# Optimization experiments

Measured on AMD Instinct MI355X. Metric: run time of the kernel, lower is better.

The kernel has to match this reference:

```python
import jax, jax.numpy as jnp
import numpy as np

N_POINTS = 2_000_000
N_BATCH = 8


def cart2polar(xyz):
    rho = jnp.sqrt(xyz[:, 0] ** 2 + xyz[:, 1] ** 2)
    phi = jnp.arctan2(xyz[:, 1], xyz[:, 0])
    return jnp.stack((rho, phi, xyz[:, 2]), axis=1)


def setup_inputs() -> dict:
    key = jax.random.key(0)
    k1, k2, k3, k4 = jax.random.split(key, 4)
    xy = jax.random.uniform(k1, (N_POINTS, 2), minval=-50.0, maxval=50.0)
    z = jax.random.uniform(k2, (N_POINTS, 1), minval=-4.0, maxval=2.0)
    inten = jax.random.uniform(k3, (N_POINTS, 1))
    points = jnp.concatenate([xy, z, inten], axis=1)  # [N, 4]
    batch_idx = jnp.sort(jax.random.randint(k4, (N_POINTS,), 0, N_BATCH)).astype(jnp.int32)
    coors_range_xyz = jnp.array([[0.0, 50.0], [-np.pi, np.pi], [-4.0, 2.0]], dtype=jnp.float32)
    spatial_shape = np.array([480, 360, 32])  # static
    scale_list = np.array([2, 4, 1])          # module appends 1; static
    return dict(points=points, batch_idx=batch_idx,
                coors_range_xyz=coors_range_xyz,
                spatial_shape=spatial_shape, scale_list=scale_list)


def _unique_rows(bxyz, dims):
    # Encode [b, gx, gy, gz] rows into a single int32 key (max 8*480*360*32 ~ 44M).
    key = ((bxyz[:, 0] * dims[0] + bxyz[:, 1]) * dims[1] + bxyz[:, 2]) * dims[2] + bxyz[:, 3]
    order = jnp.argsort(key)
    sk = key[order]
    flags = jnp.concatenate([jnp.ones((1,), bool), sk[1:] != sk[:-1]])
    rank = jnp.cumsum(flags.astype(jnp.int32)) - 1          # unique-id per sorted row
    inv = jnp.zeros_like(rank).at[order].set(rank)           # inverse map, like torch.unique
    # first occurrence of each unique row (all rows with same rank are identical)
    unq = jnp.zeros_like(bxyz).at[rank].set(bxyz[order])     # padded to [N, 4]
    num_unique = rank[-1] + 1
    return unq, inv, num_unique


def reference(points, batch_idx, coors_range_xyz, spatial_shape, scale_list):
    pc = points[:, :3]
    xyz_pol = cart2polar(pc)
    lo = coors_range_xyz[:, 0]
    hi = coors_range_xyz[:, 1]
    crop = hi - lo
    ss_np = np.asarray(spatial_shape)
    outs = []
    for scale in [int(s) for s in np.asarray(scale_list)]:
        cells = jnp.asarray(np.ceil(ss_np / scale) - 1.0, dtype=xyz_pol.dtype)
        grid = jnp.floor((jnp.clip(xyz_pol, lo, hi) - lo) / crop * cells).astype(jnp.int32)
        bxyz = jnp.concatenate([batch_idx[:, None].astype(jnp.int32), grid], axis=1)  # [N,4]
        dims = np.ceil(ss_np / scale).astype(np.int64)
        unq, inv, num = _unique_rows(bxyz, dims)
        # reorder unique coords as [b, z, y, x], cast int32 (torch: unq[:, [0,3,2,1]])
        coors = jnp.concatenate([unq[:, 0:1], unq[:, 3:4], unq[:, 2:3], unq[:, 1:2]], axis=1).astype(jnp.int32)
        outs.extend([bxyz, inv, coors, num])
    return tuple(outs)
```

## Files before the change

kernel.cpp:

```cpp
#include <hip/hip_runtime.h>
#include <cstdint>

#define DI __device__ __forceinline__

constexpr int NPTS       = 2000000;
constexpr int STRIDE_OUT = 18000001;
constexpr int OFF_INV    = 8000000;
constexpr int OFF_COORS  = 10000000;
constexpr int OFF_NUM    = 18000000;

constexpr int R2W  = 172800;
constexpr int R4W  = 21600;
constexpr int R1W  = 1382400;
constexpr int RW0  = 0;
constexpr int RW1  = R2W;
constexpr int RW2  = R2W + R4W;
constexpr int WTOT = R2W + R4W + R1W;
constexpr int NB1  = (WTOT + 1023) / 1024;
constexpr int J2   = 8;

constexpr int NBLK_INV   = (NPTS + 255) / 256;
constexpr int NBLK_COORS = (WTOT + 255) / 256;
constexpr int NBLK_TAIL  = (3 * NPTS + 255) / 256;

DI float fmul_s(float a, float b){ float r; asm("v_mul_f32 %0, %1, %2" : "=v"(r) : "v"(a), "v"(b)); return r; }
DI float fadd_s(float a, float b){ float r; asm("v_add_f32 %0, %1, %2" : "=v"(r) : "v"(a), "v"(b)); return r; }

DI void compute_keys(float x, float y, float z, int b, int (&key)[3], int (&g0)[3], int (&g1)[3], int (&g2)[3]) {
  const float PI_F     = 3.14159265358979323846f;
  const float TWO_PI_F = 6.28318530717958647692f;
  float rho = sqrtf(fadd_s(fmul_s(x, x), fmul_s(y, y)));
  float phi = atan2f(y, x);
  float tr = (fminf(fmaxf(rho, 0.0f), 50.0f) - 0.0f) / 50.0f;
  float tp = (fminf(fmaxf(phi, -PI_F), PI_F) + PI_F) / TWO_PI_F;
  float tz = (fminf(fmaxf(z, -4.0f), 2.0f) + 4.0f) / 6.0f;
  constexpr float C0[3] = {239.f, 119.f, 479.f};
  constexpr float C1[3] = {179.f,  89.f, 359.f};
  constexpr float C2[3] = { 15.f,   7.f,  31.f};
  constexpr int   D0[3] = {240, 120, 480};
  constexpr int   D1[3] = {180,  90, 360};
  constexpr int   D2[3] = { 16,   8,  32};
  #pragma unroll
  for (int s = 0; s < 3; ++s) {
    int a0 = (int)floorf(tr * C0[s]);
    int a1 = (int)floorf(tp * C1[s]);
    int a2 = (int)floorf(tz * C2[s]);
    g0[s] = a0; g1[s] = a1; g2[s] = a2;
    key[s] = ((b * D0[s] + a0) * D1[s] + a1) * D2[s] + a2;
  }
}

DI int lower_bound(const int* __restrict__ a, int n, int v) {
  int lo = 0, hi = n;
  while (lo < hi) { int m = (lo + hi) >> 1; if (a[m] < v) lo = m + 1; else hi = m; }
  return lo;
}

__global__ __launch_bounds__(256) void pass_points(const float4* __restrict__ pts,
                                                   const int* __restrict__ batch, int n,
                                                   int* __restrict__ keys,
                                                   int* __restrict__ out) {
  int i = blockIdx.x * 256 + threadIdx.x;
  if (i >= n) return;
  float4 p = pts[i];
  int b = batch[i];
  int key[3], g0[3], g1[3], g2[3];
  compute_keys(p.x, p.y, p.z, b, key, g0, g1, g2);
  #pragma unroll
  for (int s = 0; s < 3; ++s)
    *reinterpret_cast<int4*>(out + s * STRIDE_OUT + i * 4) = make_int4(b, g0[s], g1[s], g2[s]);
  keys[i] = key[0]; keys[n + i] = key[1]; keys[2 * n + i] = key[2];
}

__global__ __launch_bounds__(1024) void hist_all(const int* __restrict__ batch,
                                                 const int* __restrict__ keys, int n,
                                                 uint32_t* __restrict__ rep2s,
                                                 uint32_t* __restrict__ rep4s,
                                                 uint32_t* __restrict__ rep1s, int j1) {
  alignas(16) __shared__ uint32_t bmA[21600];
  alignas(16) __shared__ uint32_t bmB[2700];
  int t = threadIdx.x;
  if ((int)blockIdx.x < 64) {
    int bv = blockIdx.x >> 3, j = blockIdx.x & 7;
    for (int w = t * 4; w < 21600; w += 4096) *reinterpret_cast<uint4*>(bmA + w) = make_uint4(0,0,0,0);
    for (int w = t; w < 2700; w += 1024) bmB[w] = 0;
    __syncthreads();
    int lo = lower_bound(batch, n, bv);
    int hi = lower_bound(batch, n, bv + 1);
    int sz = hi - lo;
    int s = lo + (int)((long long)sz * j / J2);
    int e = lo + (int)((long long)sz * (j + 1) / J2);
    const int* k0 = keys;
    const int* k1 = keys + n;
    for (int i = s + t; i < e; i += 1024) {
      int ink2 = k0[i] - bv * 691200;
      int ink4 = k1[i] - bv * 86400;
      atomicOr(&bmA[ink2 >> 5], 1u << (ink2 & 31));
      atomicOr(&bmB[ink4 >> 5], 1u << (ink4 & 31));
    }
    __syncthreads();
    uint32_t* d2 = rep2s + (size_t)j * R2W + bv * 21600;
    uint32_t* d4 = rep4s + (size_t)j * R4W + bv * 2700;
    for (int w = t * 4; w < 21600; w += 4096) *reinterpret_cast<uint4*>(d2 + w) = *reinterpret_cast<uint4*>(bmA + w);
    for (int w = t * 4; w < 2700; w += 4096) *reinterpret_cast<uint4*>(d4 + w) = *reinterpret_cast<uint4*>(bmB + w);
  } else {
    int idx = blockIdx.x - 64;
    int j = idx >> 6;
    int slice = idx & 63;
    int bv = slice >> 3, r = slice & 7;
    for (int w = t * 4; w < 21600; w += 4096) *reinterpret_cast<uint4*>(bmA + w) = make_uint4(0,0,0,0);
    __syncthreads();
    int lo = lower_bound(batch, n, bv);
    int hi = lower_bound(batch, n, bv + 1);
    int sz = hi - lo;
    int s = lo + (int)((long long)sz * j / j1);
    int e = lo + (int)((long long)sz * (j + 1) / j1);
    const int* k2 = keys + 2 * n;
    int base = bv * 5529600 + r * 691200;
    for (int i = s + t; i < e; i += 1024) {
      int rel = k2[i] - base;
      if ((unsigned)rel < 691200u) atomicOr(&bmA[rel >> 5], 1u << (rel & 31));
    }
    __syncthreads();
    uint32_t* d = rep1s + (size_t)j * R1W + (size_t)slice * 21600;
    for (int w = t * 4; w < 21600; w += 4096) *reinterpret_cast<uint4*>(d + w) = *reinterpret_cast<uint4*>(bmA + w);
  }
}

DI uint4 merged_words(int base, const uint32_t* __restrict__ rep2s,
                      const uint32_t* __restrict__ rep4s,
                      const uint32_t* __restrict__ rep1s, int j1) {
  uint4 acc = make_uint4(0, 0, 0, 0);
  if (base < RW1) {
    #pragma unroll
    for (int c = 0; c < J2; ++c) {
      uint4 w = *reinterpret_cast<const uint4*>(rep2s + (size_t)c * R2W + base);
      acc.x |= w.x; acc.y |= w.y; acc.z |= w.z; acc.w |= w.w;
    }
  } else if (base < RW2) {
    int l = base - RW1;
    #pragma unroll
    for (int c = 0; c < J2; ++c) {
      uint4 w = *reinterpret_cast<const uint4*>(rep4s + (size_t)c * R4W + l);
      acc.x |= w.x; acc.y |= w.y; acc.z |= w.z; acc.w |= w.w;
    }
  } else {
    int l = base - RW2;
    for (int c = 0; c < j1; ++c) {
      uint4 w = *reinterpret_cast<const uint4*>(rep1s + (size_t)c * R1W + l);
      acc.x |= w.x; acc.y |= w.y; acc.z |= w.z; acc.w |= w.w;
    }
  }
  return acc;
}

__global__ __launch_bounds__(256) void scanA(const uint32_t* __restrict__ rep2s,
                                             const uint32_t* __restrict__ rep4s,
                                             const uint32_t* __restrict__ rep1s, int j1,
                                             uint32_t* __restrict__ bits,
                                             uint32_t* __restrict__ blockSums) {
  __shared__ uint32_t lds[256];
  int t = threadIdx.x;
  int base = blockIdx.x * 1024 + t * 4;
  uint32_t s = 0;
  if (base < WTOT) {
    uint4 m = merged_words(base, rep2s, rep4s, rep1s, j1);
    *reinterpret_cast<uint4*>(bits + base) = m;
    s = __popc(m.x) + __popc(m.y) + __popc(m.z) + __popc(m.w);
  }
  lds[t] = s; __syncthreads();
  for (int off = 128; off > 0; off >>= 1) { if (t < off) lds[t] += lds[t + off]; __syncthreads(); }
  if (t == 0) blockSums[blockIdx.x] = lds[0];
}

__global__ __launch_bounds__(256) void scanB(uint32_t* __restrict__ blockSums,
                                             uint32_t* __restrict__ totals, int nb) {
  __shared__ uint32_t lds[256];
  int t = threadIdx.x;
  uint32_t local[7]; uint32_t sum = 0;
  #pragma unroll
  for (int k = 0; k < 7; ++k) { int idx = t * 7 + k; uint32_t v = (idx < nb) ? blockSums[idx] : 0u; local[k] = v; sum += v; }
  lds[t] = sum; __syncthreads();
  for (int off = 1; off < 256; off <<= 1) {
    uint32_t x = (t >= off) ? lds[t - off] : 0u; __syncthreads();
    lds[t] += x; __syncthreads();
  }
  uint32_t run = lds[t] - sum;
  #pragma unroll
  for (int k = 0; k < 7; ++k) { int idx = t * 7 + k; if (idx < nb) blockSums[idx] = run; run += local[k]; }
  if (t == 255) totals[0] = run;
}

__global__ __launch_bounds__(256) void scanC(const uint32_t* __restrict__ bits,
                                             const uint32_t* __restrict__ blockSums,
                                             uint2* __restrict__ pairs) {
  __shared__ uint32_t lds[256];
  int t = threadIdx.x;
  int base = blockIdx.x * 1024 + t * 4;
  uint32_t b[4] = {0,0,0,0}; uint32_t c[4]; uint32_t sum = 0;
  if (base < WTOT) {
    uint4 w = *reinterpret_cast<const uint4*>(bits + base);
    b[0] = w.x; b[1] = w.y; b[2] = w.z; b[3] = w.w;
  }
  #pragma unroll
  for (int k = 0; k < 4; ++k) { c[k] = __popc(b[k]); sum += c[k]; }
  lds[t] = sum; __syncthreads();
  for (int off = 1; off < 256; off <<= 1) {
    uint32_t x = (t >= off) ? lds[t - off] : 0u; __syncthreads();
    lds[t] += x; __syncthreads();
  }
  uint32_t excl = lds[t] - sum + blockSums[blockIdx.x];
  if (base < WTOT) {
    #pragma unroll
    for (int k = 0; k < 4; ++k) { pairs[base + k] = make_uint2(b[k], excl); excl += c[k]; }
  }
}

template <int S>
DI void coors_word(int wi_local, uint32_t bits, uint32_t rank, int* __restrict__ coors) {
  constexpr int D0[3] = {240, 120, 480};
  constexpr int D1[3] = {180,  90, 360};
  constexpr int D2[3] = { 16,   8,  32};
  int keybase = wi_local * 32;
  while (bits) {
    int j = __builtin_ctz(bits);
    bits &= bits - 1;
    int key = keybase + j;
    int gz = key & (D2[S] - 1);
    int r  = key / D2[S];
    int q  = r / D1[S];
    int gy = r - q * D1[S];
    int bq = q / D0[S];
    int gx = q - bq * D0[S];
    *reinterpret_cast<int4*>(coors + (size_t)rank * 4) = make_int4(bq, gz, gy, gx);
    ++rank;
  }
}

__global__ __launch_bounds__(256) void epilogue(int n, const uint2* __restrict__ pairs,
                                                const uint32_t* __restrict__ totals,
                                                const int* __restrict__ keys,
                                                int* __restrict__ out) {
  int b = blockIdx.x;
  int t = threadIdx.x;
  if (b < NBLK_INV) {
    int i = b * 256 + t;
    if (i >= n) return;
    int key[3] = { keys[i], keys[n + i], keys[2 * n + i] };
    constexpr int RW[3] = {RW0, RW1, RW2};
    #pragma unroll
    for (int s = 0; s < 3; ++s) {
      uint2 pr = pairs[RW[s] + (key[s] >> 5)];
      uint32_t base = pr.y - ((s == 0) ? 0u : pairs[RW[s]].y);
      int rank = (int)(base + __popc(pr.x & ((1u << (key[s] & 31)) - 1u)));
      out[s * STRIDE_OUT + OFF_INV + i] = rank;
    }
  } else if (b < NBLK_INV + NBLK_COORS) {
    int wi = (b - NBLK_INV) * 256 + t;
    if (wi >= WTOT) return;
    uint2 pr = pairs[wi];
    if (!pr.x) return;
    if (wi < RW1) {
      coors_word<0>(wi, pr.x, pr.y, out + 0 * STRIDE_OUT + OFF_COORS);
    } else if (wi < RW2) {
      coors_word<1>(wi - RW1, pr.x, pr.y - pairs[RW1].y, out + 1 * STRIDE_OUT + OFF_COORS);
    } else {
      coors_word<2>(wi - RW2, pr.x, pr.y - pairs[RW2].y, out + 2 * STRIDE_OUT + OFF_COORS);
    }
  } else {
    int idx = (b - NBLK_INV - NBLK_COORS) * 256 + t;
    int s = 0, i = idx;
    if (i >= 2 * n)      { s = 2; i -= 2 * n; }
    else if (i >= n)     { s = 1; i -= n; }
    if (idx >= 3 * n) return;
    uint32_t lo = (s == 0) ? 0u : pairs[(s == 1) ? RW1 : RW2].y;
    uint32_t hi = (s == 0) ? pairs[RW1].y : (s == 1) ? pairs[RW2].y : totals[0];
    uint32_t num = hi - lo;
    if (i == 0) out[s * STRIDE_OUT + OFF_NUM] = (int)num;
    if ((uint32_t)i >= num)
      *reinterpret_cast<int4*>(out + s * STRIDE_OUT + OFF_COORS + (size_t)i * 4) = make_int4(0, 0, 0, 0);
  }
}

extern "C" void kernel_launch(void* const* d_in, const int* in_sizes, int n_in,
                              void* d_out, int out_size, void* d_ws, size_t ws_size,
                              hipStream_t stream) {
  const float4* pts   = (const float4*)d_in[0];
  const int*    batch = (const int*)d_in[1];
  int n = in_sizes[1];
  int* out = (int*)d_out;

  size_t base_words = (size_t)J2 * R2W + (size_t)J2 * R4W + (size_t)WTOT +
                      2 * (size_t)WTOT + NB1 + 16 + (size_t)3 * n;
  int j1 = 4;
  while (j1 > 1 && (base_words + (size_t)j1 * R1W) * 4 > ws_size) j1 >>= 1;

  uint32_t* rep2s     = (uint32_t*)d_ws;
  uint32_t* rep4s     = rep2s + (size_t)J2 * R2W;
  uint32_t* rep1s     = rep4s + (size_t)J2 * R4W;
  uint32_t* bits      = rep1s + (size_t)j1 * R1W;
  uint2*    pairs     = (uint2*)(bits + WTOT);
  uint32_t* blockSums = (uint32_t*)(pairs + WTOT);
  uint32_t* totals    = blockSums + NB1;
  int*      keys      = (int*)(totals + 16);

  int nblk = (n + 255) / 256;
  pass_points<<<nblk, 256, 0, stream>>>(pts, batch, n, keys, out);
  hist_all<<<64 + 64 * j1, 1024, 0, stream>>>(batch, keys, n, rep2s, rep4s, rep1s, j1);
  scanA<<<NB1, 256, 0, stream>>>(rep2s, rep4s, rep1s, j1, bits, blockSums);
  scanB<<<1, 256, 0, stream>>>(blockSums, totals, NB1);
  scanC<<<NB1, 256, 0, stream>>>(bits, blockSums, pairs);
  epilogue<<<NBLK_INV + NBLK_COORS + NBLK_TAIL, 256, 0, stream>>>(n, pairs, totals, keys, out);
}
```

Before: 373.3 us.

## Defer bxyz writes to epilogue, drop scanB, retile scale-1 histogram

The first pass now writes only the packed keys. The epilogue decodes the per-point [b,gx,gy,gz] rows from those keys, so the first kernel no longer writes 96 MB of coordinate output. The single-block scanB is removed: each scanC block sums the preceding block totals itself, and the final count comes from the last pair. The scale-1 histogram uses 6 larger LDS slices per batch with a fixed 4-way split, giving 256 blocks total; this changes occupancy and the number of redundant key scans.

```diff
diff --git a/kernel.cpp b/kernel.cpp
--- a/kernel.cpp
+++ b/kernel.cpp
@@ -18,6 +18,10 @@
 constexpr int WTOT = R2W + R4W + R1W;
 constexpr int NB1  = (WTOT + 1023) / 1024;
 constexpr int J2   = 8;
+constexpr int P1   = 6;
+constexpr int J1   = 4;
+constexpr int S1W  = 28800;
+constexpr int S1BITS = S1W * 32;
 
 constexpr int NBLK_INV   = (NPTS + 255) / 256;
 constexpr int NBLK_COORS = (WTOT + 255) / 256;
@@ -26,7 +30,7 @@
 DI float fmul_s(float a, float b){ float r; asm("v_mul_f32 %0, %1, %2" : "=v"(r) : "v"(a), "v"(b)); return r; }
 DI float fadd_s(float a, float b){ float r; asm("v_add_f32 %0, %1, %2" : "=v"(r) : "v"(a), "v"(b)); return r; }
 
-DI void compute_keys(float x, float y, float z, int b, int (&key)[3], int (&g0)[3], int (&g1)[3], int (&g2)[3]) {
+DI void compute_keys(float x, float y, float z, int b, int (&key)[3]) {
   const float PI_F     = 3.14159265358979323846f;
   const float TWO_PI_F = 6.28318530717958647692f;
   float rho = sqrtf(fadd_s(fmul_s(x, x), fmul_s(y, y)));
@@ -45,7 +49,6 @@
     int a0 = (int)floorf(tr * C0[s]);
     int a1 = (int)floorf(tp * C1[s]);
     int a2 = (int)floorf(tz * C2[s]);
-    g0[s] = a0; g1[s] = a1; g2[s] = a2;
     key[s] = ((b * D0[s] + a0) * D1[s] + a1) * D2[s] + a2;
   }
 }
@@ -56,19 +59,14 @@
   return lo;
 }
 
-__global__ __launch_bounds__(256) void pass_points(const float4* __restrict__ pts,
-                                                   const int* __restrict__ batch, int n,
-                                                   int* __restrict__ keys,
-                                                   int* __restrict__ out) {
+__global__ __launch_bounds__(256) void pass_keys(const float4* __restrict__ pts,
+                                                 const int* __restrict__ batch, int n,
+                                                 int* __restrict__ keys) {
   int i = blockIdx.x * 256 + threadIdx.x;
   if (i >= n) return;
   float4 p = pts[i];
-  int b = batch[i];
-  int key[3], g0[3], g1[3], g2[3];
-  compute_keys(p.x, p.y, p.z, b, key, g0, g1, g2);
-  #pragma unroll
-  for (int s = 0; s < 3; ++s)
-    *reinterpret_cast<int4*>(out + s * STRIDE_OUT + i * 4) = make_int4(b, g0[s], g1[s], g2[s]);
+  int key[3];
+  compute_keys(p.x, p.y, p.z, batch[i], key);
   keys[i] = key[0]; keys[n + i] = key[1]; keys[2 * n + i] = key[2];
 }
 
@@ -76,8 +74,8 @@
                                                  const int* __restrict__ keys, int n,
                                                  uint32_t* __restrict__ rep2s,
                                                  uint32_t* __restrict__ rep4s,
-                                                 uint32_t* __restrict__ rep1s, int j1) {
-  alignas(16) __shared__ uint32_t bmA[21600];
+                                                 uint32_t* __restrict__ rep1s) {
+  alignas(16) __shared__ uint32_t bmA[S1W];
   alignas(16) __shared__ uint32_t bmB[2700];
   int t = threadIdx.x;
   if ((int)blockIdx.x < 64) {
@@ -105,31 +103,31 @@
     for (int w = t * 4; w < 2700; w += 4096) *reinterpret_cast<uint4*>(d4 + w) = *reinterpret_cast<uint4*>(bmB + w);
   } else {
     int idx = blockIdx.x - 64;
-    int j = idx >> 6;
-    int slice = idx & 63;
-    int bv = slice >> 3, r = slice & 7;
-    for (int w = t * 4; w < 21600; w += 4096) *reinterpret_cast<uint4*>(bmA + w) = make_uint4(0,0,0,0);
+    int j = idx / 48;
+    int slice = idx - j * 48;
+    int bv = slice / 6, r = slice - bv * 6;
+    for (int w = t * 4; w < S1W; w += 4096) *reinterpret_cast<uint4*>(bmA + w) = make_uint4(0,0,0,0);
     __syncthreads();
     int lo = lower_bound(batch, n, bv);
     int hi = lower_bound(batch, n, bv + 1);
     int sz = hi - lo;
-    int s = lo + (int)((long long)sz * j / j1);
-    int e = lo + (int)((long long)sz * (j + 1) / j1);
+    int s = lo + (int)((long long)sz * j / J1);
+    int e = lo + (int)((long long)sz * (j + 1) / J1);
     const int* k2 = keys + 2 * n;
-    int base = bv * 5529600 + r * 691200;
+    int base = bv * 5529600 + r * S1BITS;
     for (int i = s + t; i < e; i += 1024) {
       int rel = k2[i] - base;
-      if ((unsigned)rel < 691200u) atomicOr(&bmA[rel >> 5], 1u << (rel & 31));
-    }
-    __syncthreads();
-    uint32_t* d = rep1s + (size_t)j * R1W + (size_t)slice * 21600;
-    for (int w = t * 4; w < 21600; w += 4096) *reinterpret_cast<uint4*>(d + w) = *reinterpret_cast<uint4*>(bmA + w);
+      if ((unsigned)rel < (unsigned)S1BITS) atomicOr(&bmA[rel >> 5], 1u << (rel & 31));
+    }
+    __syncthreads();
+    uint32_t* d = rep1s + (size_t)j * R1W + (size_t)slice * S1W;
+    for (int w = t * 4; w < S1W; w += 4096) *reinterpret_cast<uint4*>(d + w) = *reinterpret_cast<uint4*>(bmA + w);
   }
 }
 
 DI uint4 merged_words(int base, const uint32_t* __restrict__ rep2s,
                       const uint32_t* __restrict__ rep4s,
-                      const uint32_t* __restrict__ rep1s, int j1) {
+                      const uint32_t* __restrict__ rep1s) {
   uint4 acc = make_uint4(0, 0, 0, 0);
   if (base < RW1) {
     #pragma unroll
@@ -146,7 +144,8 @@
     }
   } else {
     int l = base - RW2;
-    for (int c = 0; c < j1; ++c) {
+    #pragma unroll
+    for (int c = 0; c < J1; ++c) {
       uint4 w = *reinterpret_cast<const uint4*>(rep1s + (size_t)c * R1W + l);
       acc.x |= w.x; acc.y |= w.y; acc.z |= w.z; acc.w |= w.w;
     }
@@ -156,7 +155,7 @@
 
 __global__ __launch_bounds__(256) void scanA(const uint32_t* __restrict__ rep2s,
                                              const uint32_t* __restrict__ rep4s,
-                                             const uint32_t* __restrict__ rep1s, int j1,
+                                             const uint32_t* __restrict__ rep1s,
                                              uint32_t* __restrict__ bits,
                                              uint32_t* __restrict__ blockSums) {
   __shared__ uint32_t lds[256];
@@ -164,31 +163,13 @@
   int base = blockIdx.x * 1024 + t * 4;
   uint32_t s = 0;
   if (base < WTOT) {
-    uint4 m = merged_words(base, rep2s, rep4s, rep1s, j1);
+    uint4 m = merged_words(base, rep2s, rep4s, rep1s);
     *reinterpret_cast<uint4*>(bits + base) = m;
     s = __popc(m.x) + __popc(m.y) + __popc(m.z) + __popc(m.w);
   }
   lds[t] = s; __syncthreads();
   for (int off = 128; off > 0; off >>= 1) { if (t < off) lds[t] += lds[t + off]; __syncthreads(); }
   if (t == 0) blockSums[blockIdx.x] = lds[0];
-}
-
-__global__ __launch_bounds__(256) void scanB(uint32_t* __restrict__ blockSums,
-                                             uint32_t* __restrict__ totals, int nb) {
-  __shared__ uint32_t lds[256];
-  int t = threadIdx.x;
-  uint32_t local[7]; uint32_t sum = 0;
-  #pragma unroll
-  for (int k = 0; k < 7; ++k) { int idx = t * 7 + k; uint32_t v = (idx < nb) ? blockSums[idx] : 0u; local[k] = v; sum += v; }
-  lds[t] = sum; __syncthreads();
-  for (int off = 1; off < 256; off <<= 1) {
-    uint32_t x = (t >= off) ? lds[t - off] : 0u; __syncthreads();
-    lds[t] += x; __syncthreads();
-  }
-  uint32_t run = lds[t] - sum;
-  #pragma unroll
-  for (int k = 0; k < 7; ++k) { int idx = t * 7 + k; if (idx < nb) blockSums[idx] = run; run += local[k]; }
-  if (t == 255) totals[0] = run;
 }
 
 __global__ __launch_bounds__(256) void scanC(const uint32_t* __restrict__ bits,
@@ -196,6 +177,12 @@
                                              uint2* __restrict__ pairs) {
   __shared__ uint32_t lds[256];
   int t = threadIdx.x;
+  uint32_t bs = 0;
+  for (int k = t; k < (int)blockIdx.x; k += 256) bs += blockSums[k];
+  lds[t] = bs; __syncthreads();
+  for (int off = 128; off > 0; off >>= 1) { if (t < off) lds[t] += lds[t + off]; __syncthreads(); }
+  uint32_t blockBase = lds[0];
+  __syncthreads();
   int base = blockIdx.x * 1024 + t * 4;
   uint32_t b[4] = {0,0,0,0}; uint32_t c[4]; uint32_t sum = 0;
   if (base < WTOT) {
@@ -209,7 +196,7 @@
     uint32_t x = (t >= off) ? lds[t - off] : 0u; __syncthreads();
     lds[t] += x; __syncthreads();
   }
-  uint32_t excl = lds[t] - sum + blockSums[blockIdx.x];
+  uint32_t excl = lds[t] - sum + blockBase;
   if (base < WTOT) {
     #pragma unroll
     for (int k = 0; k < 4; ++k) { pairs[base + k] = make_uint2(b[k], excl); excl += c[k]; }
@@ -217,28 +204,32 @@
 }
 
 template <int S>
-DI void coors_word(int wi_local, uint32_t bits, uint32_t rank, int* __restrict__ coors) {
+DI int4 decode_key(int key) {
   constexpr int D0[3] = {240, 120, 480};
   constexpr int D1[3] = {180,  90, 360};
   constexpr int D2[3] = { 16,   8,  32};
+  int a2 = key & (D2[S] - 1);
+  int r  = key / D2[S];
+  int q  = r / D1[S];
+  int a1 = r - q * D1[S];
+  int b  = q / D0[S];
+  int a0 = q - b * D0[S];
+  return make_int4(b, a0, a1, a2);
+}
+
+template <int S>
+DI void coors_word(int wi_local, uint32_t bits, uint32_t rank, int* __restrict__ coors) {
   int keybase = wi_local * 32;
   while (bits) {
     int j = __builtin_ctz(bits);
     bits &= bits - 1;
-    int key = keybase + j;
-    int gz = key & (D2[S] - 1);
-    int r  = key / D2[S];
-    int q  = r / D1[S];
-    int gy = r - q * D1[S];
-    int bq = q / D0[S];
-    int gx = q - bq * D0[S];
-    *reinterpret_cast<int4*>(coors + (size_t)rank * 4) = make_int4(bq, gz, gy, gx);
+    int4 d = decode_key<S>(keybase + j);
+    *reinterpret_cast<int4*>(coors + (size_t)rank * 4) = make_int4(d.x, d.w, d.z, d.y);
     ++rank;
   }
 }
 
 __global__ __launch_bounds__(256) void epilogue(int n, const uint2* __restrict__ pairs,
-                                                const uint32_t* __restrict__ totals,
                                                 const int* __restrict__ keys,
                                                 int* __restrict__ out) {
   int b = blockIdx.x;
@@ -248,6 +239,9 @@
     if (i >= n) return;
     int key[3] = { keys[i], keys[n + i], keys[2 * n + i] };
     constexpr int RW[3] = {RW0, RW1, RW2};
+    *reinterpret_cast<int4*>(out + 0 * STRIDE_OUT + i * 4) = decode_key<0>(key[0]);
+    *reinterpret_cast<int4*>(out + 1 * STRIDE_OUT + i * 4) = decode_key<1>(key[1]);
+    *reinterpret_cast<int4*>(out + 2 * STRIDE_OUT + i * 4) = decode_key<2>(key[2]);
     #pragma unroll
     for (int s = 0; s < 3; ++s) {
       uint2 pr = pairs[RW[s] + (key[s] >> 5)];
@@ -260,21 +254,19 @@
     if (wi >= WTOT) return;
     uint2 pr = pairs[wi];
     if (!pr.x) return;
-    if (wi < RW1) {
-      coors_word<0>(wi, pr.x, pr.y, out + 0 * STRIDE_OUT + OFF_COORS);
-    } else if (wi < RW2) {
-      coors_word<1>(wi - RW1, pr.x, pr.y - pairs[RW1].y, out + 1 * STRIDE_OUT + OFF_COORS);
-    } else {
-      coors_word<2>(wi - RW2, pr.x, pr.y - pairs[RW2].y, out + 2 * STRIDE_OUT + OFF_COORS);
-    }
+    if (wi < RW1)      coors_word<0>(wi,       pr.x, pr.y,                 out + 0 * STRIDE_OUT + OFF_COORS);
+    else if (wi < RW2) coors_word<1>(wi - RW1, pr.x, pr.y - pairs[RW1].y,  out + 1 * STRIDE_OUT + OFF_COORS);
+    else               coors_word<2>(wi - RW2, pr.x, pr.y - pairs[RW2].y,  out + 2 * STRIDE_OUT + OFF_COORS);
   } else {
     int idx = (b - NBLK_INV - NBLK_COORS) * 256 + t;
+    if (idx >= 3 * n) return;
     int s = 0, i = idx;
-    if (i >= 2 * n)      { s = 2; i -= 2 * n; }
-    else if (i >= n)     { s = 1; i -= n; }
-    if (idx >= 3 * n) return;
+    if (i >= 2 * n)  { s = 2; i -= 2 * n; }
+    else if (i >= n) { s = 1; i -= n; }
+    uint2 last = pairs[WTOT - 1];
+    uint32_t total = last.y + (uint32_t)__popc(last.x);
     uint32_t lo = (s == 0) ? 0u : pairs[(s == 1) ? RW1 : RW2].y;
-    uint32_t hi = (s == 0) ? pairs[RW1].y : (s == 1) ? pairs[RW2].y : totals[0];
+    uint32_t hi = (s == 0) ? pairs[RW1].y : (s == 1) ? pairs[RW2].y : total;
     uint32_t num = hi - lo;
     if (i == 0) out[s * STRIDE_OUT + OFF_NUM] = (int)num;
     if ((uint32_t)i >= num)
@@ -290,25 +282,18 @@
   int n = in_sizes[1];
   int* out = (int*)d_out;
 
-  size_t base_words = (size_t)J2 * R2W + (size_t)J2 * R4W + (size_t)WTOT +
-                      2 * (size_t)WTOT + NB1 + 16 + (size_t)3 * n;
-  int j1 = 4;
-  while (j1 > 1 && (base_words + (size_t)j1 * R1W) * 4 > ws_size) j1 >>= 1;
-
   uint32_t* rep2s     = (uint32_t*)d_ws;
   uint32_t* rep4s     = rep2s + (size_t)J2 * R2W;
   uint32_t* rep1s     = rep4s + (size_t)J2 * R4W;
-  uint32_t* bits      = rep1s + (size_t)j1 * R1W;
+  uint32_t* bits      = rep1s + (size_t)J1 * R1W;
   uint2*    pairs     = (uint2*)(bits + WTOT);
   uint32_t* blockSums = (uint32_t*)(pairs + WTOT);
-  uint32_t* totals    = blockSums + NB1;
-  int*      keys      = (int*)(totals + 16);
+  int*      keys      = (int*)(blockSums + NB1 + 16);
 
   int nblk = (n + 255) / 256;
-  pass_points<<<nblk, 256, 0, stream>>>(pts, batch, n, keys, out);
-  hist_all<<<64 + 64 * j1, 1024, 0, stream>>>(batch, keys, n, rep2s, rep4s, rep1s, j1);
-  scanA<<<NB1, 256, 0, stream>>>(rep2s, rep4s, rep1s, j1, bits, blockSums);
-  scanB<<<1, 256, 0, stream>>>(blockSums, totals, NB1);
+  pass_keys<<<nblk, 256, 0, stream>>>(pts, batch, n, keys);
+  hist_all<<<256, 1024, 0, stream>>>(batch, keys, n, rep2s, rep4s, rep1s);
+  scanA<<<NB1, 256, 0, stream>>>(rep2s, rep4s, rep1s, bits, blockSums);
   scanC<<<NB1, 256, 0, stream>>>(bits, blockSums, pairs);
-  epilogue<<<NBLK_INV + NBLK_COORS + NBLK_TAIL, 256, 0, stream>>>(n, pairs, totals, keys, out);
-}
+  epilogue<<<NBLK_INV + NBLK_COORS + NBLK_TAIL, 256, 0, stream>>>(n, pairs, keys, out);
+}
```

New measurement: 345.6 us. 7.4% less time.
